# Kernel tuning notes

Hardware: AMD Instinct MI355X
Metric: run time of the kernel (lower is better)

Reference implementation:

```python
import math
import jax, jax.numpy as jnp
import numpy as np

B, H, SQ, SKV, DM = 4, 16, 1024, 1024, 1024
K = 17  # k+1 relative slots
DK = DM // H


def setup_inputs() -> dict:
    key = jax.random.key(0)
    ks = jax.random.split(key, 14)
    n = jax.random.normal
    w_scale = 1.0 / math.sqrt(DM)
    return {
        "query": n(ks[0], (B, SQ, DM), jnp.float32),
        "key": n(ks[1], (B, SKV, DM), jnp.float32),
        "value": n(ks[2], (B, SKV, DM), jnp.float32),
        "pos_enc": n(ks[3], (B, H, K, SKV), jnp.float32),
        "pos_pad": n(ks[4], (B, H, K, SKV), jnp.float32),
        "cross_pos_enc": n(ks[5], (B, H, K, SQ), jnp.float32),
        "cross_pos_pad": n(ks[6], (B, H, K, SQ), jnp.float32),
        "rel_q": n(ks[7], (1, H, 2 * K, DK), jnp.float32) * 0.02,
        "rel_k": n(ks[8], (1, H, 2 * K, DK), jnp.float32) * 0.02,
        "rel_v": n(ks[9], (1, H, 2 * K, DK), jnp.float32) * 0.02,
        "Wq": n(ks[10], (DM, DM), jnp.float32) * w_scale,
        "Wk": n(ks[11], (DM, DM), jnp.float32) * w_scale,
        "Wv": n(ks[12], (DM, DM), jnp.float32) * w_scale,
        "Wo": n(ks[13], (DM, DM), jnp.float32) * w_scale,
    }


def _heads(x, W):
    # nn.Linear(bias=False): y = x @ W.T, then transpose_for_scores -> [B,H,S,DK]
    y = x @ W.T
    b, s, _ = y.shape
    return y.reshape(b, s, H, DK).transpose(0, 2, 1, 3)


def reference(query, key, value, pos_enc, pos_pad, cross_pos_enc, cross_pos_pad,
              rel_q, rel_k, rel_v, Wq, Wk, Wv, Wo):
    q = _heads(query, Wq)   # [B,H,SQ,DK]
    k = _heads(key, Wk)     # [B,H,SKV,DK]
    v = _heads(value, Wv)   # [B,H,SKV,DK]

    # split rel tables: first K rows pair with *_enc, last K rows with *_pad
    rk_e, rk_p = rel_k[0, :, :K], rel_k[0, :, K:]
    rq_e, rq_p = rel_q[0, :, :K], rel_q[0, :, K:]
    rv_e, rv_p = rel_v[0, :, :K], rel_v[0, :, K:]

    # content scores + rel-position bias terms, all [B,H,SQ,SKV]
    scores = jnp.einsum('bhqd,bhsd->bhqs', q, k)
    scores += jnp.einsum('bhqd,hrd,bhrs->bhqs', q, rk_e, pos_enc)
    scores += jnp.einsum('bhqd,hrd,bhrs->bhqs', q, rk_p, pos_pad)
    scores += jnp.einsum('bhsd,hrd,bhrq->bhqs', k, rq_e, cross_pos_enc)
    scores += jnp.einsum('bhsd,hrd,bhrq->bhqs', k, rq_p, cross_pos_pad)

    attn = jax.nn.softmax(scores / math.sqrt(DK), axis=-1)

    out = jnp.einsum('bhqs,bhsd->bhqd', attn, v)
    out += jnp.einsum('bhqs,bhrs,hrd->bhqd', attn, pos_enc, rv_e)
    out += jnp.einsum('bhqs,bhrs,hrd->bhqd', attn, pos_pad, rv_p)

    # finalize_output: merge heads then out_proj
    out = out.transpose(0, 2, 1, 3).reshape(B, SQ, DM)
    return out @ Wo.T
```

## Files before the change

kernel.cpp:

```cpp
#include <hip/hip_runtime.h>
#include <hip/hip_bf16.h>
#include <stdint.h>

typedef float f32x4 __attribute__((ext_vector_type(4)));
typedef __bf16 bf16x8 __attribute__((ext_vector_type(8)));

#define NBH 64
#define SS 1024
#define DAUG 160
#define KAPPA 0.18033688011104293f

static __device__ __forceinline__ unsigned short f2b(float f) {
  union { float f; uint32_t u; } v; v.f = f;
  return (unsigned short)((v.u + 0x7fffu + ((v.u >> 16) & 1u)) >> 16);
}
static __device__ __forceinline__ float b2f(unsigned short s) {
  union { uint32_t u; float f; } v; v.u = ((uint32_t)s) << 16;
  return v.f;
}

static __device__ __forceinline__ void async16(const void* g, void* l) {
  __builtin_amdgcn_global_load_lds(
      (const __attribute__((address_space(1))) uint32_t*)g,
      (__attribute__((address_space(3))) uint32_t*)l, 16, 0, 0);
}

template <int CTRL>
static __device__ __forceinline__ float dppmaxstep(float x) {
  int y = __builtin_amdgcn_update_dpp(__builtin_bit_cast(int, x), __builtin_bit_cast(int, x),
                                      CTRL, 0xF, 0xF, false);
  return fmaxf(x, __builtin_bit_cast(float, y));
}
static __device__ __forceinline__ float rowmax16(float x) {
  x = dppmaxstep<0x128>(x);
  x = dppmaxstep<0x124>(x);
  x = dppmaxstep<0x122>(x);
  x = dppmaxstep<0x121>(x);
  return x;
}

__global__ void convert7(const float* q, const float* k, const float* v,
                         const float* wq, const float* wk, const float* wv, const float* wo,
                         unsigned short* xq, unsigned short* xk, unsigned short* xv,
                         unsigned short* bwq, unsigned short* bwk, unsigned short* bwv,
                         unsigned short* bwo) {
  const float* s; unsigned short* d; int n;
  switch (blockIdx.y) {
    case 0: s = q;  d = xq;  n = 4194304; break;
    case 1: s = k;  d = xk;  n = 4194304; break;
    case 2: s = v;  d = xv;  n = 4194304; break;
    case 3: s = wq; d = bwq; n = 1048576; break;
    case 4: s = wk; d = bwk; n = 1048576; break;
    case 5: s = wv; d = bwv; n = 1048576; break;
    default: s = wo; d = bwo; n = 1048576; break;
  }
  int n4 = n >> 2;
  for (int i = blockIdx.x * blockDim.x + threadIdx.x; i < n4; i += gridDim.x * blockDim.x) {
    float4 f = ((const float4*)s)[i];
    ushort4 o;
    o.x = f2b(f.x); o.y = f2b(f.y); o.z = f2b(f.z); o.w = f2b(f.w);
    ((ushort4*)d)[i] = o;
  }
}

__global__ __launch_bounds__(256) void proj_qkv(
    const unsigned short* __restrict__ Xq, const unsigned short* __restrict__ Xk,
    const unsigned short* __restrict__ Xv, const unsigned short* __restrict__ Wqb,
    const unsigned short* __restrict__ Wkb, const unsigned short* __restrict__ Wvb,
    unsigned short* __restrict__ Qt, unsigned short* __restrict__ Kt,
    unsigned short* __restrict__ Vp, const float* __restrict__ relk,
    const float* __restrict__ relq) {
  const int n_ = blockIdx.x + 32 * (blockIdx.y + 8 * blockIdx.z);
  const int o_ = (n_ & 7) * 96 + (n_ >> 3);
  const int bx = o_ & 31, by = (o_ >> 5) & 7, z = o_ >> 8;

  const unsigned short* A = (z == 0) ? Xq : (z == 1) ? Xk : Xv;
  const unsigned short* Bw = (z == 0) ? Wqb : (z == 1) ? Wkb : Wvb;
  unsigned short* Dst = (z == 0) ? Qt : (z == 1) ? Kt : Vp;
  const int dstride = (z == 2) ? 64 : DAUG;
  const float sc = (z == 0) ? KAPPA : 1.0f;

  __shared__ unsigned short SMEM[23296];
  unsigned short* AtB = SMEM;
  unsigned short* BtB = SMEM + 8192;
  unsigned short* RelL = SMEM + 16384;
  unsigned short* Ys = SMEM;

  const int tid = threadIdx.x, wave = tid >> 6, lane = tid & 63;
  const int r15 = lane & 15, g4 = lane >> 4;
  const int i0 = bx * 128, j0 = by * 128;
  const int wm = (wave >> 1) * 64, wn = (wave & 1) * 64;

  if (z < 2) {
    const float* rel = (z == 0) ? relk : relq;
    const int h0 = by * 2;
    for (int idx = tid; idx < 2 * 48 * 64; idx += 256) {
      int hh = idx / (48 * 64), rem = idx % (48 * 64);
      int r = rem >> 6, d = rem & 63;
      float v = (r < 34) ? rel[(((size_t)(h0 + hh)) * 34 + r) * 64 + d] : 0.f;
      RelL[(hh * 48 + r) * 72 + d] = f2b(v);
    }
  }

  auto stage = [&](int k0, int buf) {
#pragma unroll
    for (int c = 0; c < 2; ++c) {
      int ch = (wave * 2 + c) * 64 + lane;
      int row = ch >> 2, cg = ch & 3;
      async16(A + (size_t)(i0 + row) * 1024 + k0 + cg * 8, AtB + buf * 4096 + (wave * 2 + c) * 512);
      async16(Bw + (size_t)(j0 + row) * 1024 + k0 + cg * 8, BtB + buf * 4096 + (wave * 2 + c) * 512);
    }
  };

  f32x4 acc[4][4];
#pragma unroll
  for (int m = 0; m < 4; ++m)
#pragma unroll
    for (int n = 0; n < 4; ++n) acc[m][n] = (f32x4){0.f, 0.f, 0.f, 0.f};

  stage(0, 0);
  __syncthreads();

  for (int it = 0; it < 32; ++it) {
    const int cur = it & 1, nxt = cur ^ 1;
    if (it < 31) stage((it + 1) * 32, nxt);
    bf16x8 af[4], bf[4];
#pragma unroll
    for (int m = 0; m < 4; ++m)
      af[m] = *(const bf16x8*)(AtB + cur * 4096 + (wm + m * 16 + r15) * 32 + g4 * 8);
#pragma unroll
    for (int n = 0; n < 4; ++n)
      bf[n] = *(const bf16x8*)(BtB + cur * 4096 + (wn + n * 16 + r15) * 32 + g4 * 8);
    __builtin_amdgcn_s_setprio(1);
#pragma unroll
    for (int m = 0; m < 4; ++m)
#pragma unroll
      for (int n = 0; n < 4; ++n)
        acc[m][n] = __builtin_amdgcn_mfma_f32_16x16x32_bf16(af[m], bf[n], acc[m][n], 0, 0, 0);
    __builtin_amdgcn_s_setprio(0);
    __syncthreads();
  }

#pragma unroll
  for (int m = 0; m < 4; ++m)
#pragma unroll
    for (int n = 0; n < 4; ++n)
#pragma unroll
      for (int r = 0; r < 4; ++r) {
        int lrow = wm + m * 16 + g4 * 4 + r;
        int lcol = wn + n * 16 + r15;
        int i = i0 + lrow, j = j0 + lcol;
        float y = acc[m][n][r] * sc;
        int b = i >> 10, s = i & 1023, h = j >> 6, d = j & 63;
        Dst[(((size_t)b * 16 + h) * SS + s) * dstride + d] = f2b(y);
        if (z < 2) {
          int c8 = (lcol >> 3) ^ (lrow & 7);
          Ys[lrow * 128 + c8 * 8 + (lcol & 7)] = f2b(y);
        }
      }

  if (z < 2) {
    const int cbase = (z == 0) ? 64 : 98;
    __syncthreads();
#pragma unroll
    for (int hh = 0; hh < 2; ++hh) {
      bf16x8 bfr[3][2];
#pragma unroll
      for (int n = 0; n < 3; ++n)
#pragma unroll
        for (int st = 0; st < 2; ++st)
          bfr[n][st] = *(const bf16x8*)(RelL + (hh * 48 + n * 16 + r15) * 72 + st * 32 + g4 * 8);

      f32x4 a2[2][3];
#pragma unroll
      for (int m2 = 0; m2 < 2; ++m2)
#pragma unroll
        for (int n = 0; n < 3; ++n) a2[m2][n] = (f32x4){0.f, 0.f, 0.f, 0.f};

#pragma unroll
      for (int m2 = 0; m2 < 2; ++m2) {
        int lrow = wave * 32 + m2 * 16 + r15;
        int c8a = (hh * 8 + 0 * 4 + g4) ^ (lrow & 7);
        int c8b = (hh * 8 + 1 * 4 + g4) ^ (lrow & 7);
        bf16x8 a0 = *(const bf16x8*)(Ys + lrow * 128 + c8a * 8);
        bf16x8 a1 = *(const bf16x8*)(Ys + lrow * 128 + c8b * 8);
#pragma unroll
        for (int n = 0; n < 3; ++n) {
          a2[m2][n] = __builtin_amdgcn_mfma_f32_16x16x32_bf16(a0, bfr[n][0], a2[m2][n], 0, 0, 0);
          a2[m2][n] = __builtin_amdgcn_mfma_f32_16x16x32_bf16(a1, bfr[n][1], a2[m2][n], 0, 0, 0);
        }
      }

      const int h = by * 2 + hh;
#pragma unroll
      for (int m2 = 0; m2 < 2; ++m2)
#pragma unroll
        for (int n = 0; n < 3; ++n) {
          int col = n * 16 + r15;
          if (col < 34) {
#pragma unroll
            for (int rr = 0; rr < 4; ++rr) {
              int i = i0 + wave * 32 + m2 * 16 + g4 * 4 + rr;
              int b = i >> 10, s = i & 1023;
              Dst[(((size_t)b * 16 + h) * SS + s) * DAUG + cbase + col] = f2b(a2[m2][n][rr]);
            }
          }
        }
    }
  }
}

__global__ __launch_bounds__(256) void gemm_out(const unsigned short* __restrict__ Oh,
                                                const unsigned short* __restrict__ Wob,
                                                float* __restrict__ Out) {
  const int n_ = blockIdx.x + 32 * blockIdx.y;
  const int o_ = (n_ & 7) * 32 + (n_ >> 3);
  const int bx = o_ & 31, by = o_ >> 5;

  __shared__ unsigned short At[2][128 * 32];
  __shared__ unsigned short Bt[2][128 * 32];

  const int tid = threadIdx.x, wave = tid >> 6, lane = tid & 63;
  const int r15 = lane & 15, g4 = lane >> 4;
  const int i0 = bx * 128, j0 = by * 128;
  const int wm = (wave >> 1) * 64, wn = (wave & 1) * 64;

  auto stage = [&](int k0, int buf) {
#pragma unroll
    for (int c = 0; c < 2; ++c) {
      int ch = (wave * 2 + c) * 64 + lane;
      int row = ch >> 2, cg = ch & 3;
      int i = i0 + row, b = i >> 10, s = i & 1023;
      int kcol = k0 + cg * 8, h = kcol >> 6, dd = kcol & 63;
      async16(Oh + (((size_t)b * 16 + h) * SS + s) * 64 + dd, &At[buf][0] + (wave * 2 + c) * 512);
      async16(Wob + (size_t)(j0 + row) * 1024 + k0 + cg * 8, &Bt[buf][0] + (wave * 2 + c) * 512);
    }
  };

  f32x4 acc[4][4];
#pragma unroll
  for (int m = 0; m < 4; ++m)
#pragma unroll
    for (int n = 0; n < 4; ++n) acc[m][n] = (f32x4){0.f, 0.f, 0.f, 0.f};

  stage(0, 0);
  __syncthreads();

  for (int it = 0; it < 32; ++it) {
    const int cur = it & 1, nxt = cur ^ 1;
    if (it < 31) stage((it + 1) * 32, nxt);
    bf16x8 af[4], bf[4];
#pragma unroll
    for (int m = 0; m < 4; ++m)
      af[m] = *(const bf16x8*)(&At[cur][(wm + m * 16 + r15) * 32 + g4 * 8]);
#pragma unroll
    for (int n = 0; n < 4; ++n)
      bf[n] = *(const bf16x8*)(&Bt[cur][(wn + n * 16 + r15) * 32 + g4 * 8]);
    __builtin_amdgcn_s_setprio(1);
#pragma unroll
    for (int m = 0; m < 4; ++m)
#pragma unroll
      for (int n = 0; n < 4; ++n)
        acc[m][n] = __builtin_amdgcn_mfma_f32_16x16x32_bf16(af[m], bf[n], acc[m][n], 0, 0, 0);
    __builtin_amdgcn_s_setprio(0);
    __syncthreads();
  }

#pragma unroll
  for (int m = 0; m < 4; ++m)
#pragma unroll
    for (int n = 0; n < 4; ++n)
#pragma unroll
      for (int r = 0; r < 4; ++r) {
        int i = i0 + wm + m * 16 + g4 * 4 + r;
        int j = j0 + wn + n * 16 + r15;
        Out[(size_t)i * 1024 + j] = acc[m][n][r];
      }
}

__global__ __launch_bounds__(256) void pos_vp(unsigned short* __restrict__ Qt,
                                              unsigned short* __restrict__ Kt,
                                              const float* __restrict__ cpe,
                                              const float* __restrict__ cpp,
                                              const float* __restrict__ pe,
                                              const float* __restrict__ pp,
                                              const unsigned short* __restrict__ Vp,
                                              const float* __restrict__ relv,
                                              unsigned short* __restrict__ VpT) {
  const int z = blockIdx.z;
  unsigned short* T = z ? Kt : Qt;
  const float* Pe = z ? pe : cpe;
  const float* Pp = z ? pp : cpp;
  const int cbase = z ? 64 : 98;
  const float scale = z ? 1.0f : KAPPA;
  const int bh = blockIdx.y, h = bh & 15, s0 = blockIdx.x * 64;
  const int tid = threadIdx.x;
  __shared__ float PeL[17][65];
  __shared__ float PpL[17][65];
  __shared__ unsigned short VT[64][72];

  for (int idx = tid; idx < 17 * 64; idx += 256) {
    int r = idx >> 6, c = idx & 63;
    PeL[r][c] = Pe[((size_t)bh * 17 + r) * SS + s0 + c];
    PpL[r][c] = Pp[((size_t)bh * 17 + r) * SS + s0 + c];
  }
  __syncthreads();

  for (int idx = tid; idx < 4096; idx += 256) {
    int s = idx >> 6, j = idx & 63;
    if (j < 34) {
      float v = (j < 17) ? PeL[j][s] : PpL[j - 17][s];
      T[((size_t)bh * SS + s0 + s) * DAUG + cbase + j] = f2b(v * scale);
    } else if (j < 62) {
      T[((size_t)bh * SS + s0 + s) * DAUG + 132 + (j - 34)] = 0;
    }
  }

  if (z == 1) {
    const int d = tid & 63, sg = tid >> 6;
    float acc[16];
#pragma unroll
    for (int si = 0; si < 16; ++si) acc[si] = 0.f;
    for (int r = 0; r < 17; ++r) {
      float ve = relv[((size_t)h * 34 + r) * 64 + d];
      float vpv = relv[((size_t)h * 34 + 17 + r) * 64 + d];
#pragma unroll
      for (int si = 0; si < 16; ++si) {
        int s = sg * 16 + si;
        acc[si] += PeL[r][s] * ve + PpL[r][s] * vpv;
      }
    }
#pragma unroll
    for (int si = 0; si < 16; ++si) {
      int s = sg * 16 + si;
      float v = b2f(Vp[((size_t)bh * SS + s0 + s) * 64 + d]) + acc[si];
      VT[d][s] = f2b(v);
    }
    __syncthreads();

    for (int c = tid; c < 512; c += 256) {
      int row = c >> 3, c8 = c & 7;
      uint4 v = *(const uint4*)&VT[row][c8 * 8];
      *(uint4*)(VpT + ((size_t)bh * 80 + row) * 1024 + s0 + c8 * 8) = v;
    }
    if (tid < 128) {
      int row = 64 + (tid >> 3), c8 = tid & 7;
      uint32_t w = (row == 64) ? 0x3F803F80u : 0u;
      uint4 v = {w, w, w, w};
      *(uint4*)(VpT + ((size_t)bh * 80 + row) * 1024 + s0 + c8 * 8) = v;
    }
  }
}

__global__ __launch_bounds__(512, 4) void flash_attn3(
    const unsigned short* __restrict__ Qt, const unsigned short* __restrict__ Kt,
    const unsigned short* __restrict__ VpT, unsigned short* __restrict__ Oh) {
  const int bh = blockIdx.y;
  const int q0 = blockIdx.x * 128;
  const int tid = threadIdx.x, wave = tid >> 6, lane = tid & 63;
  const int r15 = lane & 15, g4 = lane >> 4;

  __shared__ unsigned short Ks[2][64 * 160];
  __shared__ unsigned short Vs[2][80 * 64];
  __shared__ unsigned short Ps[128 * 72];

  const unsigned short* Kbase = Kt + (size_t)bh * SS * DAUG;
  const unsigned short* Vbase = VpT + (size_t)bh * 80 * 1024;

  bf16x8 qf[5];
  {
    const unsigned short* Qg = Qt + ((size_t)bh * SS + q0 + wave * 16 + r15) * DAUG;
#pragma unroll
    for (int kk = 0; kk < 5; ++kk) qf[kk] = *(const bf16x8*)(Qg + kk * 32 + g4 * 8);
  }

  auto stageK = [&](int kv0, int buf) {
    const unsigned short* Kg = Kbase + (size_t)kv0 * DAUG;
#pragma unroll
    for (int j = 0; j < 2; ++j) {
      int ibase = j * 512 + wave * 64;
      int i = ibase + lane;
      int row = i / 20, c = i % 20;
      int cs = (c < 16) ? (c ^ (row & 7)) : (16 + ((c & 3) ^ (row & 3)));
      async16(Kg + (size_t)row * DAUG + cs * 8, &Ks[buf][0] + (size_t)ibase * 8);
    }
    if (wave < 4) {
      int ibase = 1024 + wave * 64;
      int i = ibase + lane;
      int row = i / 20, c = i % 20;
      int cs = (c < 16) ? (c ^ (row & 7)) : (16 + ((c & 3) ^ (row & 3)));
      async16(Kg + (size_t)row * DAUG + cs * 8, &Ks[buf][0] + (size_t)ibase * 8);
    }
  };
  auto stageV = [&](int kv0, int buf) {
    {
      int c = tid;
      int row = c >> 3, c8 = c & 7;
      async16(Vbase + (size_t)row * 1024 + kv0 + ((c8 ^ (row & 7)) << 3),
              &Vs[buf][0] + (size_t)c * 8);
    }
    if (tid < 128) {
      int c = 512 + tid;
      int row = c >> 3, c8 = c & 7;
      async16(Vbase + (size_t)row * 1024 + kv0 + ((c8 ^ (row & 7)) << 3),
              &Vs[buf][0] + (size_t)c * 8);
    }
  };

  stageK(0, 0);
  stageV(0, 0);
  __syncthreads();

  f32x4 accO[5];
#pragma unroll
  for (int df = 0; df < 5; ++df) accO[df] = (f32x4){0.f, 0.f, 0.f, 0.f};
  float run_m[4] = {-INFINITY, -INFINITY, -INFINITY, -INFINITY};

  for (int t = 0; t < 16; ++t) {
    const int cur = t & 1, nxt = cur ^ 1;
    if (t < 15) {
      stageK((t + 1) * 64, nxt);
      stageV((t + 1) * 64, nxt);
    }

    f32x4 s[4];
#pragma unroll
    for (int f = 0; f < 4; ++f) s[f] = (f32x4){0.f, 0.f, 0.f, 0.f};
    __builtin_amdgcn_s_setprio(1);
#pragma unroll
    for (int f = 0; f < 4; ++f) {
      int row = f * 16 + r15;
#pragma unroll
      for (int kk = 0; kk < 5; ++kk) {
        int c = kk * 4 + g4;
        int cs = (c < 16) ? (c ^ (row & 7)) : (16 + ((c & 3) ^ (row & 3)));
        bf16x8 kf = *(const bf16x8*)(&Ks[cur][(size_t)row * DAUG + cs * 8]);
        s[f] = __builtin_amdgcn_mfma_f32_16x16x32_bf16(qf[kk], kf, s[f], 0, 0, 0);
      }
    }
    __builtin_amdgcn_s_setprio(0);

    float mx[4];
#pragma unroll
    for (int r = 0; r < 4; ++r)
      mx[r] = rowmax16(fmaxf(fmaxf(s[0][r], s[1][r]), fmaxf(s[2][r], s[3][r])));

    bool stable = (mx[0] <= run_m[0] + 8.f) && (mx[1] <= run_m[1] + 8.f) &&
                  (mx[2] <= run_m[2] + 8.f) && (mx[3] <= run_m[3] + 8.f);
    if (!__all(stable)) {
#pragma unroll
      for (int r = 0; r < 4; ++r) {
        float mnew = fmaxf(run_m[r], mx[r]);
        float corr = exp2f(run_m[r] - mnew);
        run_m[r] = mnew;
#pragma unroll
        for (int df = 0; df < 5; ++df) accO[df][r] *= corr;
      }
    }
#pragma unroll
    for (int r = 0; r < 4; ++r)
#pragma unroll
      for (int f = 0; f < 4; ++f) s[f][r] = exp2f(s[f][r] - run_m[r]);

#pragma unroll
    for (int f = 0; f < 4; ++f)
#pragma unroll
      for (int r = 0; r < 4; ++r)
        ((__bf16*)Ps)[(wave * 16 + g4 * 4 + r) * 72 + f * 16 + r15] = (__bf16)s[f][r];

    __builtin_amdgcn_s_setprio(1);
#pragma unroll
    for (int ks = 0; ks < 2; ++ks) {
      bf16x8 pa = *(const bf16x8*)(Ps + (wave * 16 + r15) * 72 + ks * 32 + g4 * 8);
#pragma unroll
      for (int df = 0; df < 5; ++df) {
        int row = df * 16 + r15;
        bf16x8 vb = *(const bf16x8*)(&Vs[cur][(size_t)row * 64 + (((ks * 4 + g4) ^ (r15 & 7)) << 3)]);
        accO[df] = __builtin_amdgcn_mfma_f32_16x16x32_bf16(pa, vb, accO[df], 0, 0, 0);
      }
    }
    __builtin_amdgcn_s_setprio(0);

    __syncthreads();
  }

  float rl[4];
#pragma unroll
  for (int r = 0; r < 4; ++r) {
    float l = __shfl(accO[4][r], lane & 48, 64);
    rl[r] = 1.f / l;
  }
#pragma unroll
  for (int df = 0; df < 4; ++df)
#pragma unroll
    for (int r = 0; r < 4; ++r) {
      float o = accO[df][r] * rl[r];
      Oh[((size_t)bh * SS + q0 + wave * 16 + g4 * 4 + r) * 64 + df * 16 + r15] = f2b(o);
    }
}

extern "C" void kernel_launch(void* const* d_in, const int* in_sizes, int n_in,
                              void* d_out, int out_size, void* d_ws, size_t ws_size,
                              hipStream_t stream) {
  const float* query = (const float*)d_in[0];
  const float* key = (const float*)d_in[1];
  const float* value = (const float*)d_in[2];
  const float* pe = (const float*)d_in[3];
  const float* pp = (const float*)d_in[4];
  const float* cpe = (const float*)d_in[5];
  const float* cpp = (const float*)d_in[6];
  const float* relq = (const float*)d_in[7];
  const float* relk = (const float*)d_in[8];
  const float* relv = (const float*)d_in[9];
  const float* Wq = (const float*)d_in[10];
  const float* Wk = (const float*)d_in[11];
  const float* Wv = (const float*)d_in[12];
  const float* Wo = (const float*)d_in[13];
  float* out = (float*)d_out;
  char* ws = (char*)d_ws;

  unsigned short* Xq = (unsigned short*)(ws + 0);
  unsigned short* Xk = (unsigned short*)(ws + 8388608);
  unsigned short* Xv = (unsigned short*)(ws + 16777216);
  unsigned short* Wqb = (unsigned short*)(ws + 25165824);
  unsigned short* Wkb = (unsigned short*)(ws + 27262976);
  unsigned short* Wvb = (unsigned short*)(ws + 29360128);
  unsigned short* Wob = (unsigned short*)(ws + 31457280);
  unsigned short* Qt = (unsigned short*)(ws + 33554432);
  unsigned short* Kt = (unsigned short*)(ws + 54525952);
  unsigned short* Vp = (unsigned short*)(ws + 75497472);
  unsigned short* Oh = (unsigned short*)(ws + 0);
  unsigned short* VpT = (unsigned short*)(ws + 8388608);

  convert7<<<dim3(1024, 7, 1), 256, 0, stream>>>(query, key, value, Wq, Wk, Wv, Wo, Xq, Xk, Xv,
                                                 Wqb, Wkb, Wvb, Wob);
  proj_qkv<<<dim3(32, 8, 3), 256, 0, stream>>>(Xq, Xk, Xv, Wqb, Wkb, Wvb, Qt, Kt, Vp, relk, relq);
  pos_vp<<<dim3(16, 64, 2), 256, 0, stream>>>(Qt, Kt, cpe, cpp, pe, pp, Vp, relv, VpT);
  flash_attn3<<<dim3(8, 64, 1), 512, 0, stream>>>(Qt, Kt, VpT, Oh);
  gemm_out<<<dim3(32, 8, 1), 256, 0, stream>>>(Oh, Wob, out);
}
```

Before: 173.0 us.

## Rewrite flash attention with 32x32 MFMA, register P, and split-KV waves

The attention kernel now uses 32x32x16 bf16 MFMAs and computes S transposed (K as A operand), so the softmax row max becomes a per-lane reduction plus one cross-half shuffle. P is repacked into B-operand fragments with shuffles instead of going through LDS. Each 64-key tile is split between two wave groups, whose partial outputs are merged through LDS at the end. The ones-row trick in V for the row sum is dropped in favour of an explicit running sum, which shrinks VpT to 64 rows. The trade-off is an extra end-of-kernel merge with two barriers and higher register pressure from the larger accumulators.

```diff
diff --git a/kernel.cpp b/kernel.cpp
--- a/kernel.cpp
+++ b/kernel.cpp
@@ -3,6 +3,7 @@
 #include <stdint.h>
 
 typedef float f32x4 __attribute__((ext_vector_type(4)));
+typedef float f32x16 __attribute__((ext_vector_type(16)));
 typedef __bf16 bf16x8 __attribute__((ext_vector_type(8)));
 
 #define NBH 64
@@ -18,6 +19,9 @@
   union { uint32_t u; float f; } v; v.u = ((uint32_t)s) << 16;
   return v.f;
 }
+static __device__ __forceinline__ uint32_t pk2(float a, float b) {
+  return (uint32_t)f2b(a) | ((uint32_t)f2b(b) << 16);
+}
 
 static __device__ __forceinline__ void async16(const void* g, void* l) {
   __builtin_amdgcn_global_load_lds(
@@ -25,18 +29,8 @@
       (__attribute__((address_space(3))) uint32_t*)l, 16, 0, 0);
 }
 
-template <int CTRL>
-static __device__ __forceinline__ float dppmaxstep(float x) {
-  int y = __builtin_amdgcn_update_dpp(__builtin_bit_cast(int, x), __builtin_bit_cast(int, x),
-                                      CTRL, 0xF, 0xF, false);
-  return fmaxf(x, __builtin_bit_cast(float, y));
-}
-static __device__ __forceinline__ float rowmax16(float x) {
-  x = dppmaxstep<0x128>(x);
-  x = dppmaxstep<0x124>(x);
-  x = dppmaxstep<0x122>(x);
-  x = dppmaxstep<0x121>(x);
-  return x;
+static __device__ __forceinline__ int ksw(int c, int row) {
+  return (c < 16) ? (c ^ (row & 7)) : (16 + ((c & 3) ^ (row & 3)));
 }
 
 __global__ void convert7(const float* q, const float* k, const float* v,
@@ -341,37 +335,30 @@
     for (int c = tid; c < 512; c += 256) {
       int row = c >> 3, c8 = c & 7;
       uint4 v = *(const uint4*)&VT[row][c8 * 8];
-      *(uint4*)(VpT + ((size_t)bh * 80 + row) * 1024 + s0 + c8 * 8) = v;
-    }
-    if (tid < 128) {
-      int row = 64 + (tid >> 3), c8 = tid & 7;
-      uint32_t w = (row == 64) ? 0x3F803F80u : 0u;
-      uint4 v = {w, w, w, w};
-      *(uint4*)(VpT + ((size_t)bh * 80 + row) * 1024 + s0 + c8 * 8) = v;
-    }
-  }
-}
-
-__global__ __launch_bounds__(512, 4) void flash_attn3(
+      *(uint4*)(VpT + ((size_t)bh * 64 + row) * 1024 + s0 + c8 * 8) = v;
+    }
+  }
+}
+
+__global__ __launch_bounds__(512, 4) void flash_attn5(
     const unsigned short* __restrict__ Qt, const unsigned short* __restrict__ Kt,
     const unsigned short* __restrict__ VpT, unsigned short* __restrict__ Oh) {
   const int bh = blockIdx.y;
   const int q0 = blockIdx.x * 128;
   const int tid = threadIdx.x, wave = tid >> 6, lane = tid & 63;
-  const int r15 = lane & 15, g4 = lane >> 4;
-
-  __shared__ unsigned short Ks[2][64 * 160];
-  __shared__ unsigned short Vs[2][80 * 64];
-  __shared__ unsigned short Ps[128 * 72];
+  const int l31 = lane & 31, hi = lane >> 5;
+  const int qq = wave & 3, kvh = wave >> 2;
+
+  __shared__ unsigned short SM[28672];
 
   const unsigned short* Kbase = Kt + (size_t)bh * SS * DAUG;
-  const unsigned short* Vbase = VpT + (size_t)bh * 80 * 1024;
-
-  bf16x8 qf[5];
+  const unsigned short* Vbase = VpT + (size_t)bh * 64 * 1024;
+
+  bf16x8 qf[10];
   {
-    const unsigned short* Qg = Qt + ((size_t)bh * SS + q0 + wave * 16 + r15) * DAUG;
-#pragma unroll
-    for (int kk = 0; kk < 5; ++kk) qf[kk] = *(const bf16x8*)(Qg + kk * 32 + g4 * 8);
+    const unsigned short* Qg = Qt + ((size_t)bh * SS + q0 + qq * 32 + l31) * DAUG + hi * 8;
+#pragma unroll
+    for (int kk = 0; kk < 10; ++kk) qf[kk] = *(const bf16x8*)(Qg + kk * 16);
   }
 
   auto stageK = [&](int kv0, int buf) {
@@ -381,40 +368,32 @@
       int ibase = j * 512 + wave * 64;
       int i = ibase + lane;
       int row = i / 20, c = i % 20;
-      int cs = (c < 16) ? (c ^ (row & 7)) : (16 + ((c & 3) ^ (row & 3)));
-      async16(Kg + (size_t)row * DAUG + cs * 8, &Ks[buf][0] + (size_t)ibase * 8);
+      async16(Kg + (size_t)row * DAUG + ksw(c, row) * 8, SM + buf * 10240 + (size_t)ibase * 8);
     }
     if (wave < 4) {
       int ibase = 1024 + wave * 64;
       int i = ibase + lane;
       int row = i / 20, c = i % 20;
-      int cs = (c < 16) ? (c ^ (row & 7)) : (16 + ((c & 3) ^ (row & 3)));
-      async16(Kg + (size_t)row * DAUG + cs * 8, &Ks[buf][0] + (size_t)ibase * 8);
+      async16(Kg + (size_t)row * DAUG + ksw(c, row) * 8, SM + buf * 10240 + (size_t)ibase * 8);
     }
   };
   auto stageV = [&](int kv0, int buf) {
-    {
-      int c = tid;
-      int row = c >> 3, c8 = c & 7;
-      async16(Vbase + (size_t)row * 1024 + kv0 + ((c8 ^ (row & 7)) << 3),
-              &Vs[buf][0] + (size_t)c * 8);
-    }
-    if (tid < 128) {
-      int c = 512 + tid;
-      int row = c >> 3, c8 = c & 7;
-      async16(Vbase + (size_t)row * 1024 + kv0 + ((c8 ^ (row & 7)) << 3),
-              &Vs[buf][0] + (size_t)c * 8);
-    }
+    int c = tid;
+    int row = c >> 3, c8 = c & 7;
+    async16(Vbase + (size_t)row * 1024 + kv0 + ((c8 ^ (row & 7)) << 3),
+            SM + 20480 + buf * 4096 + (size_t)c * 8);
   };
 
   stageK(0, 0);
   stageV(0, 0);
   __syncthreads();
 
-  f32x4 accO[5];
-#pragma unroll
-  for (int df = 0; df < 5; ++df) accO[df] = (f32x4){0.f, 0.f, 0.f, 0.f};
-  float run_m[4] = {-INFINITY, -INFINITY, -INFINITY, -INFINITY};
+  f32x16 accO[2];
+#pragma unroll
+  for (int j = 0; j < 16; ++j) { accO[0][j] = 0.f; accO[1][j] = 0.f; }
+  float run_m = -INFINITY, run_l = 0.f;
+
+  const int krow = kvh * 32 + l31;
 
   for (int t = 0; t < 16; ++t) {
     const int cur = t & 1, nxt = cur ^ 1;
@@ -423,60 +402,71 @@
       stageV((t + 1) * 64, nxt);
     }
 
-    f32x4 s[4];
-#pragma unroll
-    for (int f = 0; f < 4; ++f) s[f] = (f32x4){0.f, 0.f, 0.f, 0.f};
+    f32x16 sT;
+#pragma unroll
+    for (int j = 0; j < 16; ++j) sT[j] = 0.f;
     __builtin_amdgcn_s_setprio(1);
 #pragma unroll
-    for (int f = 0; f < 4; ++f) {
-      int row = f * 16 + r15;
-#pragma unroll
-      for (int kk = 0; kk < 5; ++kk) {
-        int c = kk * 4 + g4;
-        int cs = (c < 16) ? (c ^ (row & 7)) : (16 + ((c & 3) ^ (row & 3)));
-        bf16x8 kf = *(const bf16x8*)(&Ks[cur][(size_t)row * DAUG + cs * 8]);
-        s[f] = __builtin_amdgcn_mfma_f32_16x16x32_bf16(qf[kk], kf, s[f], 0, 0, 0);
-      }
+    for (int kk = 0; kk < 10; ++kk) {
+      int c = 2 * kk + hi;
+      bf16x8 kf = *(const bf16x8*)(SM + cur * 10240 + (size_t)krow * 160 + ksw(c, krow) * 8);
+      sT = __builtin_amdgcn_mfma_f32_32x32x16_bf16(kf, qf[kk], sT, 0, 0, 0);
     }
     __builtin_amdgcn_s_setprio(0);
 
-    float mx[4];
-#pragma unroll
-    for (int r = 0; r < 4; ++r)
-      mx[r] = rowmax16(fmaxf(fmaxf(s[0][r], s[1][r]), fmaxf(s[2][r], s[3][r])));
-
-    bool stable = (mx[0] <= run_m[0] + 8.f) && (mx[1] <= run_m[1] + 8.f) &&
-                  (mx[2] <= run_m[2] + 8.f) && (mx[3] <= run_m[3] + 8.f);
-    if (!__all(stable)) {
-#pragma unroll
-      for (int r = 0; r < 4; ++r) {
-        float mnew = fmaxf(run_m[r], mx[r]);
-        float corr = exp2f(run_m[r] - mnew);
-        run_m[r] = mnew;
-#pragma unroll
-        for (int df = 0; df < 5; ++df) accO[df][r] *= corr;
-      }
-    }
-#pragma unroll
-    for (int r = 0; r < 4; ++r)
-#pragma unroll
-      for (int f = 0; f < 4; ++f) s[f][r] = exp2f(s[f][r] - run_m[r]);
-
-#pragma unroll
-    for (int f = 0; f < 4; ++f)
-#pragma unroll
-      for (int r = 0; r < 4; ++r)
-        ((__bf16*)Ps)[(wave * 16 + g4 * 4 + r) * 72 + f * 16 + r15] = (__bf16)s[f][r];
+    float mx = sT[0];
+#pragma unroll
+    for (int j = 1; j < 16; ++j) mx = fmaxf(mx, sT[j]);
+    mx = fmaxf(mx, __shfl_xor(mx, 32, 64));
+
+    bool cond = (mx <= run_m + 8.f);
+    if (!__all(cond)) {
+      float mnew = fmaxf(run_m, mx);
+      float corr = exp2f(run_m - mnew);
+      run_m = mnew;
+      run_l *= corr;
+#pragma unroll
+      for (int j = 0; j < 16; ++j) { accO[0][j] *= corr; accO[1][j] *= corr; }
+    }
+    float lsum = 0.f;
+#pragma unroll
+    for (int j = 0; j < 16; ++j) {
+      float p = exp2f(sT[j] - run_m);
+      sT[j] = p;
+      lsum += p;
+    }
+    run_l += lsum + __shfl_xor(lsum, 32, 64);
+
+    uint32_t w[8];
+#pragma unroll
+    for (int j = 0; j < 8; ++j) w[j] = pk2(sT[2 * j], sT[2 * j + 1]);
+
+    bf16x8 bfrag[2];
+#pragma unroll
+    for (int ks = 0; ks < 2; ++ks) {
+      int b = ks * 4;
+      uint32_t sel_a = hi ? w[b + 0] : w[b + 2];
+      uint32_t sel_b = hi ? w[b + 1] : w[b + 3];
+      uint32_t x_a = (uint32_t)__shfl_xor((int)sel_a, 32, 64);
+      uint32_t x_b = (uint32_t)__shfl_xor((int)sel_b, 32, 64);
+      union { uint32_t u[4]; bf16x8 v; } bw;
+      bw.u[0] = hi ? x_a : w[b + 0];
+      bw.u[1] = hi ? x_b : w[b + 1];
+      bw.u[2] = hi ? w[b + 2] : x_a;
+      bw.u[3] = hi ? w[b + 3] : x_b;
+      bfrag[ks] = bw.v;
+    }
 
     __builtin_amdgcn_s_setprio(1);
 #pragma unroll
-    for (int ks = 0; ks < 2; ++ks) {
-      bf16x8 pa = *(const bf16x8*)(Ps + (wave * 16 + r15) * 72 + ks * 32 + g4 * 8);
-#pragma unroll
-      for (int df = 0; df < 5; ++df) {
-        int row = df * 16 + r15;
-        bf16x8 vb = *(const bf16x8*)(&Vs[cur][(size_t)row * 64 + (((ks * 4 + g4) ^ (r15 & 7)) << 3)]);
-        accO[df] = __builtin_amdgcn_mfma_f32_16x16x32_bf16(pa, vb, accO[df], 0, 0, 0);
+    for (int dt = 0; dt < 2; ++dt) {
+      int vrow = dt * 32 + l31;
+#pragma unroll
+      for (int ks = 0; ks < 2; ++ks) {
+        int c = kvh * 4 + ks * 2 + hi;
+        bf16x8 vf = *(const bf16x8*)(SM + 20480 + cur * 4096 + (size_t)vrow * 64 +
+                                     ((c ^ (vrow & 7)) << 3));
+        accO[dt] = __builtin_amdgcn_mfma_f32_32x32x16_bf16(vf, bfrag[ks], accO[dt], 0, 0, 0);
       }
     }
     __builtin_amdgcn_s_setprio(0);
@@ -484,19 +474,50 @@
     __syncthreads();
   }
 
-  float rl[4];
-#pragma unroll
-  for (int r = 0; r < 4; ++r) {
-    float l = __shfl(accO[4][r], lane & 48, 64);
-    rl[r] = 1.f / l;
-  }
-#pragma unroll
-  for (int df = 0; df < 4; ++df)
-#pragma unroll
-    for (int r = 0; r < 4; ++r) {
-      float o = accO[df][r] * rl[r];
-      Oh[((size_t)bh * SS + q0 + wave * 16 + g4 * 4 + r) * 64 + df * 16 + r15] = f2b(o);
-    }
+  float* SC = (float*)SM;
+  float* Ml = SC + 8192;
+  float* Ll = SC + 8320;
+  uint32_t* OT = (uint32_t*)(SC + 8448);
+
+  if (kvh == 1) {
+#pragma unroll
+    for (int dt = 0; dt < 2; ++dt)
+#pragma unroll
+      for (int j = 0; j < 16; ++j) {
+        int d = (j & 3) + 8 * (j >> 2) + 4 * hi + 32 * dt;
+        SC[qq * 2048 + d * 32 + l31] = accO[dt][j];
+      }
+    if (hi == 0) {
+      Ml[qq * 32 + l31] = run_m;
+      Ll[qq * 32 + l31] = run_l;
+    }
+  }
+  __syncthreads();
+  if (kvh == 0) {
+    float m1 = Ml[qq * 32 + l31], l1v = Ll[qq * 32 + l31];
+    float M = fmaxf(run_m, m1);
+    float c0 = exp2f(run_m - M), c1 = exp2f(m1 - M);
+    float inv = 1.f / (run_l * c0 + l1v * c1);
+#pragma unroll
+    for (int dt = 0; dt < 2; ++dt)
+#pragma unroll
+      for (int j = 0; j < 16; j += 2) {
+        int d = (j & 3) + 8 * (j >> 2) + 4 * hi + 32 * dt;
+        float o0 = (accO[dt][j] * c0 + SC[qq * 2048 + d * 32 + l31] * c1) * inv;
+        float o1 = (accO[dt][j + 1] * c0 + SC[qq * 2048 + (d + 1) * 32 + l31] * c1) * inv;
+        OT[(qq * 32 + l31) * 33 + (d >> 1)] = pk2(o0, o1);
+      }
+  }
+  __syncthreads();
+  for (int c = tid; c < 1024; c += 512) {
+    int row = c >> 3, ch = c & 7;
+    uint4 v;
+    v.x = OT[row * 33 + ch * 4 + 0];
+    v.y = OT[row * 33 + ch * 4 + 1];
+    v.z = OT[row * 33 + ch * 4 + 2];
+    v.w = OT[row * 33 + ch * 4 + 3];
+    *(uint4*)(Oh + ((size_t)bh * SS + q0 + row) * 64 + ch * 8) = v;
+  }
 }
 
 extern "C" void kernel_launch(void* const* d_in, const int* in_sizes, int n_in,
@@ -536,6 +557,6 @@
                                                  Wqb, Wkb, Wvb, Wob);
   proj_qkv<<<dim3(32, 8, 3), 256, 0, stream>>>(Xq, Xk, Xv, Wqb, Wkb, Wvb, Qt, Kt, Vp, relk, relq);
   pos_vp<<<dim3(16, 64, 2), 256, 0, stream>>>(Qt, Kt, cpe, cpp, pe, pp, Vp, relv, VpT);
-  flash_attn3<<<dim3(8, 64, 1), 512, 0, stream>>>(Qt, Kt, VpT, Oh);
+  flash_attn5<<<dim3(8, 64, 1), 512, 0, stream>>>(Qt, Kt, VpT, Oh);
   gemm_out<<<dim3(32, 8, 1), 256, 0, stream>>>(Oh, Wob, out);
 }
```

New measurement: 168.3 us. -2.7%, faster.
